# Kernel optimization log

Hardware: AMD Instinct MI355X
Metric: run time of the kernel (lower is better)

The kernel has to match this reference:

```python
import jax, jax.numpy as jnp
import numpy as np

NEG_INF = -9e15  # mask value used by the original module
LEAKY_SLOPE = 0.2


def setup_inputs() -> dict:
    key = jax.random.key(0)
    k1, k2, k3, k4 = jax.random.split(key, 4)
    B, N, F_in = 4, 2048, 128
    H, head_dim = 4, 32
    h = jax.random.normal(k1, (B, N, F_in), dtype=jnp.float32)
    adj = jax.random.randint(k2, (N, N), 0, 2, dtype=jnp.int32)
    W = jax.random.normal(k3, (H, F_in, head_dim), dtype=jnp.float32)
    a = jax.random.normal(k4, (H, 2 * head_dim, 1), dtype=jnp.float32)
    return {"h": h, "adj": adj, "W": W, "a": a}


def reference(h, adj, W, a):
    # h: (B, N, F_in); adj: (N, N) int; W: (H, F_in, D); a: (H, 2D, 1)
    D = W.shape[-1]
    Wh = jnp.einsum('bnf,hfd->bhnd', h, W)          # (B, H, N, D)
    # Original builds [Wh_i || Wh_j] @ a. Split a so that
    # e_ij = Wh_i . a_src + Wh_j . a_dst  (identical math, no N^2*2D concat).
    a_src = a[:, :D, 0]                              # (H, D)
    a_dst = a[:, D:, 0]                              # (H, D)
    e_src = jnp.einsum('bhnd,hd->bhn', Wh, a_src)    # (B, H, N)
    e_dst = jnp.einsum('bhnd,hd->bhn', Wh, a_dst)    # (B, H, N)
    e = jax.nn.leaky_relu(e_src[..., :, None] + e_dst[..., None, :],
                          negative_slope=LEAKY_SLOPE)  # (B, H, N, N)
    masked = jnp.where(adj[None, None] > 0, e, NEG_INF)
    attn = jax.nn.softmax(masked, axis=-1)           # dropout: eval mode (identity)
    out = jnp.einsum('bhij,bhjd->bhid', attn, Wh)    # (B, H, N, D)
    B, H, N, _ = out.shape
    # concat heads along feature dim == transpose to (B, N, H, D) then merge
    return out.transpose(0, 2, 1, 3).reshape(B, N, H * D)
```

## Files before the change

### kernel.cpp

```cpp
#include <hip/hip_runtime.h>
#include <hip/hip_bf16.h>

typedef unsigned short u16;
using f32x4 = __attribute__((ext_vector_type(4))) float;
using short8 = __attribute__((ext_vector_type(8))) short;

constexpr int B_ = 4, N_ = 2048, FIN = 128, H_ = 4, D_ = 32;
constexpr int BH = B_ * H_;
constexpr float LOG2E = 1.4426950408889634f;

static __device__ __forceinline__ float bitsel(int m, float a, unsigned int bu) {
  return __uint_as_float((__float_as_uint(a) & (unsigned)m) | (bu & ~(unsigned)m));
}

constexpr int NPB = 16;

__global__ __launch_bounds__(256) void wh_kernel(
    const float* __restrict__ h, const float* __restrict__ W,
    const float* __restrict__ a, u16* __restrict__ WhT,
    float* __restrict__ es, float* __restrict__ ed) {
  __shared__ float hsh[NPB][FIN];
  __shared__ float part[NPB][H_][D_];
  const int t = threadIdx.x;
  const int fh = t >> 7, hh = (t >> 5) & 3, d = t & 31;

  float Wr[64];
#pragma unroll
  for (int ff = 0; ff < 64; ++ff)
    Wr[ff] = W[hh * (FIN * D_) + (fh * 64 + ff) * D_ + d];

  const int n0 = blockIdx.x * NPB;
  for (int idx = t; idx < NPB * FIN; idx += 256)
    hsh[idx >> 7][idx & 127] = h[(size_t)n0 * FIN + idx];
  __syncthreads();

  float accs[NPB];
#pragma unroll
  for (int r = 0; r < NPB; ++r) {
    float acc = 0.f;
    const float* hr = &hsh[r][fh * 64];
#pragma unroll
    for (int f4 = 0; f4 < 16; ++f4) {
      float4 hv = *(const float4*)(hr + f4 * 4);
      acc += hv.x * Wr[f4 * 4 + 0];
      acc += hv.y * Wr[f4 * 4 + 1];
      acc += hv.z * Wr[f4 * 4 + 2];
      acc += hv.w * Wr[f4 * 4 + 3];
    }
    accs[r] = acc;
  }
  if (fh == 0) {
#pragma unroll
    for (int r = 0; r < NPB; ++r) part[r][hh][d] = accs[r];
  }
  __syncthreads();
  if (fh == 1) {
    const int b = n0 / N_;
    const int bh = b * H_ + hh;
    const int n0r = n0 & (N_ - 1);
    const float asrc = a[hh * 2 * D_ + d];
    const float adst = a[hh * 2 * D_ + D_ + d];
    union { u16 s[16]; uint4 q[2]; } wbuf;
#pragma unroll
    for (int r = 0; r < NPB; ++r) {
      const float wh = accs[r] + part[r][hh][d];
      union { __hip_bfloat16 h; u16 u; } cv;
      cv.h = __float2bfloat16(wh);
      wbuf.s[r] = cv.u;
      float vs = wh * asrc, vd = wh * adst;
#pragma unroll
      for (int o = 16; o >= 1; o >>= 1) {
        vs += __shfl_xor(vs, o, 64);
        vd += __shfl_xor(vd, o, 64);
      }
      if (d == 0) {
        es[(size_t)bh * N_ + n0r + r] = vs * LOG2E;
        ed[(size_t)bh * N_ + n0r + r] = vd * LOG2E;
      }
    }
    u16* dst = WhT + ((size_t)(bh * 32 + d)) * N_ + n0r;
    *(uint4*)dst = wbuf.q[0];
    *(uint4*)(dst + 8) = wbuf.q[1];
  }
}

constexpr int PACKW = N_ * N_ / 64;

__global__ __launch_bounds__(256) void pack_kernel(
    const int* __restrict__ adj, unsigned long long* __restrict__ mask) {
  const int wave = (blockIdx.x * 256 + threadIdx.x) >> 6;
  const int lane = threadIdx.x & 63;
#pragma unroll
  for (int t = 0; t < 8; ++t) {
    const int wdx = wave * 8 + t;
    const int i = wdx >> 5;
    const int jb = (wdx & 31) << 6;
    const int v = adj[(size_t)i * N_ + jb + lane];
    const unsigned long long m = __ballot(v > 0);
    if (lane == 0) mask[wdx] = m;
  }
}

constexpr int ROWS = 16;
constexpr int NSTEP = 16;

__global__ __launch_bounds__(256, 8) void attn_kernel(
    const float* __restrict__ es, const float* __restrict__ ed,
    const u16* __restrict__ WhT, const unsigned int* __restrict__ mask32,
    float* __restrict__ out) {
  __shared__ __align__(16) char arena[12352];
  __shared__ float essh[ROWS], rmsh[ROWS];
  __shared__ float sumsh[4][16];

  float* edsh = (float*)arena;
  unsigned int* maskw = (unsigned int*)(arena + 8192);

  const int bh = blockIdx.x >> 7;
  const int i0 = (blockIdx.x & 127) * ROWS;
  const int tid = threadIdx.x, lane = tid & 63, w = tid >> 6;
  const int jq = w;

  const float* edb = ed + (size_t)bh * N_;
  *(float4*)&edsh[tid * 8] = *(const float4*)(edb + tid * 8);
  *(float4*)&edsh[tid * 8 + 4] = *(const float4*)(edb + tid * 8 + 4);
  const unsigned int* mrow = mask32 + (size_t)i0 * 64;
#pragma unroll
  for (int q = 0; q < 4; ++q) {
    const int idx = tid + q * 256;
    maskw[(idx >> 6) * 65 + (idx & 63)] = mrow[(idx >> 6) * 64 + (idx & 63)];
  }
  if (tid < ROWS) essh[tid] = es[(size_t)bh * N_ + i0 + tid];
  __syncthreads();

  {
    const unsigned int NEGU = __float_as_uint(-3.0e38f);
    float mx0 = -3.0e38f, mx1 = -3.0e38f, mx2 = -3.0e38f, mx3 = -3.0e38f;
    const int l31 = lane & 31, lh = lane >> 5;
#pragma unroll 8
    for (int q = 0; q < 32; ++q) {
      const float edv = edsh[q * 64 + lane];
      const int base = w * 4 * 65 + q * 2 + lh;
      const int b0 = __builtin_amdgcn_sbfe((int)maskw[base], l31, 1);
      const int b1 = __builtin_amdgcn_sbfe((int)maskw[base + 65], l31, 1);
      const int b2 = __builtin_amdgcn_sbfe((int)maskw[base + 130], l31, 1);
      const int b3 = __builtin_amdgcn_sbfe((int)maskw[base + 195], l31, 1);
      mx0 = fmaxf(mx0, bitsel(b0, edv, NEGU));
      mx1 = fmaxf(mx1, bitsel(b1, edv, NEGU));
      mx2 = fmaxf(mx2, bitsel(b2, edv, NEGU));
      mx3 = fmaxf(mx3, bitsel(b3, edv, NEGU));
    }
#pragma unroll
    for (int o = 32; o >= 1; o >>= 1) {
      mx0 = fmaxf(mx0, __shfl_xor(mx0, o, 64));
      mx1 = fmaxf(mx1, __shfl_xor(mx1, o, 64));
      mx2 = fmaxf(mx2, __shfl_xor(mx2, o, 64));
      mx3 = fmaxf(mx3, __shfl_xor(mx3, o, 64));
    }
    if (lane == 0) {
      rmsh[w * 4 + 0] = mx0;
      rmsh[w * 4 + 1] = mx1;
      rmsh[w * 4 + 2] = mx2;
      rmsh[w * 4 + 3] = mx3;
    }
  }
  __syncthreads();

  const int row16 = lane & 15, kg = lane >> 4;
  const float esr = essh[row16];
  const float xm = esr + rmsh[row16];
  const float mxr = fmaxf(xm, 0.2f * xm);
  const float cpos = esr - mxr;
  const float cneg = 0.2f * esr - mxr;

  const unsigned int* mwp = maskw + row16 * 65 + jq * 16;
  const int kg8 = kg << 3;
  unsigned int mreg[16];
#pragma unroll
  for (int s = 0; s < NSTEP; ++s) mreg[s] = mwp[s] >> kg8;

  const u16* wb0 = WhT + ((size_t)(bh * 32 + row16)) * N_ + jq * 512 + kg * 8;
  const u16* wb1 = wb0 + (size_t)16 * N_;
  const float* edq = edsh + jq * 512 + kg * 8;

  short8 ones;
#pragma unroll
  for (int q = 0; q < 8; ++q) ones[q] = (short)0x3F80;

  f32x4 c0 = {}, c1 = {}, csum = {};
  short8 b0 = *(const short8*)wb0;
  short8 b1 = *(const short8*)wb1;

#pragma unroll
  for (int s = 0; s < NSTEP; ++s) {
    const int sn = (s + 1 < NSTEP) ? (s + 1) : s;
    const short8 nb0 = *(const short8*)(wb0 + sn * 32);
    const short8 nb1 = *(const short8*)(wb1 + sn * 32);

    const unsigned int mw = mreg[s];
    const float4 ea = *(const float4*)(edq + s * 32);
    const float4 eb = *(const float4*)(edq + s * 32 + 4);
    const float ev[8] = {ea.x, ea.y, ea.z, ea.w, eb.x, eb.y, eb.z, eb.w};
    float p[8];
#pragma unroll
    for (int j = 0; j < 8; ++j) {
      const float edv = ev[j];
      const float zp = edv + cpos;
      const float zn = __builtin_fmaf(edv, 0.2f, cneg);
      const float z = fmaxf(zp, zn);
      const float e = __builtin_amdgcn_exp2f(z);
      const int mbit = __builtin_amdgcn_sbfe((int)mw, j, 1);
      p[j] = bitsel(mbit, e, 0u);
    }
    union { unsigned int u[4]; short8 v8; } af;
    asm("v_cvt_pk_bf16_f32 %0, %1, %2" : "=v"(af.u[0]) : "v"(p[0]), "v"(p[1]));
    asm("v_cvt_pk_bf16_f32 %0, %1, %2" : "=v"(af.u[1]) : "v"(p[2]), "v"(p[3]));
    asm("v_cvt_pk_bf16_f32 %0, %1, %2" : "=v"(af.u[2]) : "v"(p[4]), "v"(p[5]));
    asm("v_cvt_pk_bf16_f32 %0, %1, %2" : "=v"(af.u[3]) : "v"(p[6]), "v"(p[7]));

    c0 = __builtin_amdgcn_mfma_f32_16x16x32_bf16(af.v8, b0, c0, 0, 0, 0);
    c1 = __builtin_amdgcn_mfma_f32_16x16x32_bf16(af.v8, b1, c1, 0, 0, 0);
    csum = __builtin_amdgcn_mfma_f32_16x16x32_bf16(af.v8, ones, csum, 0, 0, 0);
    b0 = nb0;
    b1 = nb1;
  }

  __syncthreads();

  float* redc = (float*)arena;
#pragma unroll
  for (int r = 0; r < 4; ++r) {
    redc[(jq * 16 + kg * 4 + r) * 33 + row16] = c0[r];
    redc[(jq * 16 + kg * 4 + r) * 33 + 16 + row16] = c1[r];
  }
  if (row16 == 0) {
#pragma unroll
    for (int r = 0; r < 4; ++r) sumsh[jq][kg * 4 + r] = csum[r];
  }
  __syncthreads();

  if (tid < 128) {
    const int r = tid >> 3;
    const int c4 = (tid & 7) * 4;
    const float inv =
        1.f / fmaxf(sumsh[0][r] + sumsh[1][r] + sumsh[2][r] + sumsh[3][r],
                    1e-30f);
    float4 o;
    const float* p0 = &redc[(0 * 16 + r) * 33 + c4];
    const float* p1 = &redc[(1 * 16 + r) * 33 + c4];
    const float* p2 = &redc[(2 * 16 + r) * 33 + c4];
    const float* p3 = &redc[(3 * 16 + r) * 33 + c4];
    o.x = (p0[0] + p1[0] + p2[0] + p3[0]) * inv;
    o.y = (p0[1] + p1[1] + p2[1] + p3[1]) * inv;
    o.z = (p0[2] + p1[2] + p2[2] + p3[2]) * inv;
    o.w = (p0[3] + p1[3] + p2[3] + p3[3]) * inv;
    const int b = bh >> 2, hh = bh & 3;
    *(float4*)&out[((size_t)(b * N_ + i0 + r)) * (H_ * D_) + hh * 32 + c4] = o;
  }
}

extern "C" void kernel_launch(void* const* d_in, const int* in_sizes, int n_in,
                              void* d_out, int out_size, void* d_ws,
                              size_t ws_size, hipStream_t stream) {
  const float* h = (const float*)d_in[0];
  const int* adj = (const int*)d_in[1];
  const float* W = (const float*)d_in[2];
  const float* a = (const float*)d_in[3];
  char* ws = (char*)d_ws;
  u16* WhT = (u16*)ws;
  float* es = (float*)(ws + (2u << 20));
  float* ed = (float*)(ws + (2u << 20) + (128u << 10));
  unsigned long long* mask =
      (unsigned long long*)(ws + (2u << 20) + (256u << 10));
  float* out = (float*)d_out;

  wh_kernel<<<B_ * N_ / NPB, 256, 0, stream>>>(h, W, a, WhT, es, ed);
  pack_kernel<<<PACKW / (8 * 4), 256, 0, stream>>>(adj, mask);
  attn_kernel<<<BH * (N_ / ROWS), 256, 0, stream>>>(
      es, ed, WhT, (const unsigned int*)mask, out);
}
```

Baseline: 124.8 us.

## Deepen B-operand prefetch to two steps and pack score math into float2 ops

```diff
diff --git a/kernel.cpp b/kernel.cpp
--- a/kernel.cpp
+++ b/kernel.cpp
@@ -3,6 +3,7 @@
 
 typedef unsigned short u16;
 using f32x4 = __attribute__((ext_vector_type(4))) float;
+using f32x2 = __attribute__((ext_vector_type(2))) float;
 using short8 = __attribute__((ext_vector_type(8))) short;
 
 constexpr int B_ = 4, N_ = 2048, FIN = 128, H_ = 4, D_ = 32;
@@ -169,14 +170,11 @@
   const float esr = essh[row16];
   const float xm = esr + rmsh[row16];
   const float mxr = fmaxf(xm, 0.2f * xm);
-  const float cpos = esr - mxr;
-  const float cneg = 0.2f * esr - mxr;
+  const f32x2 cpos2 = {esr - mxr, esr - mxr};
+  const f32x2 cneg2 = {0.2f * esr - mxr, 0.2f * esr - mxr};
 
   const unsigned int* mwp = maskw + row16 * 65 + jq * 16;
   const int kg8 = kg << 3;
-  unsigned int mreg[16];
-#pragma unroll
-  for (int s = 0; s < NSTEP; ++s) mreg[s] = mwp[s] >> kg8;
 
   const u16* wb0 = WhT + ((size_t)(bh * 32 + row16)) * N_ + jq * 512 + kg * 8;
   const u16* wb1 = wb0 + (size_t)16 * N_;
@@ -187,29 +185,35 @@
   for (int q = 0; q < 8; ++q) ones[q] = (short)0x3F80;
 
   f32x4 c0 = {}, c1 = {}, csum = {};
-  short8 b0 = *(const short8*)wb0;
-  short8 b1 = *(const short8*)wb1;
+  short8 ba0 = *(const short8*)wb0;
+  short8 ba1 = *(const short8*)wb1;
+  short8 bb0 = *(const short8*)(wb0 + 32);
+  short8 bb1 = *(const short8*)(wb1 + 32);
 
 #pragma unroll
   for (int s = 0; s < NSTEP; ++s) {
-    const int sn = (s + 1 < NSTEP) ? (s + 1) : s;
+    const int sn = (s + 2 < NSTEP) ? (s + 2) : s;
     const short8 nb0 = *(const short8*)(wb0 + sn * 32);
     const short8 nb1 = *(const short8*)(wb1 + sn * 32);
 
-    const unsigned int mw = mreg[s];
+    const unsigned int mw = mwp[s] >> kg8;
     const float4 ea = *(const float4*)(edq + s * 32);
     const float4 eb = *(const float4*)(edq + s * 32 + 4);
-    const float ev[8] = {ea.x, ea.y, ea.z, ea.w, eb.x, eb.y, eb.z, eb.w};
+    const f32x2 ev2[4] = {{ea.x, ea.y}, {ea.z, ea.w}, {eb.x, eb.y}, {eb.z, eb.w}};
     float p[8];
 #pragma unroll
-    for (int j = 0; j < 8; ++j) {
-      const float edv = ev[j];
-      const float zp = edv + cpos;
-      const float zn = __builtin_fmaf(edv, 0.2f, cneg);
-      const float z = fmaxf(zp, zn);
-      const float e = __builtin_amdgcn_exp2f(z);
-      const int mbit = __builtin_amdgcn_sbfe((int)mw, j, 1);
-      p[j] = bitsel(mbit, e, 0u);
+    for (int jj = 0; jj < 4; ++jj) {
+      const f32x2 e2 = ev2[jj];
+      const f32x2 zp = e2 + cpos2;
+      const f32x2 zn = e2 * 0.2f + cneg2;
+      const float z0 = fmaxf(zp.x, zn.x);
+      const float z1 = fmaxf(zp.y, zn.y);
+      const float e0 = __builtin_amdgcn_exp2f(z0);
+      const float e1 = __builtin_amdgcn_exp2f(z1);
+      const int m0 = __builtin_amdgcn_sbfe((int)mw, 2 * jj, 1);
+      const int m1 = __builtin_amdgcn_sbfe((int)mw, 2 * jj + 1, 1);
+      p[2 * jj] = bitsel(m0, e0, 0u);
+      p[2 * jj + 1] = bitsel(m1, e1, 0u);
     }
     union { unsigned int u[4]; short8 v8; } af;
     asm("v_cvt_pk_bf16_f32 %0, %1, %2" : "=v"(af.u[0]) : "v"(p[0]), "v"(p[1]));
@@ -217,11 +221,11 @@
     asm("v_cvt_pk_bf16_f32 %0, %1, %2" : "=v"(af.u[2]) : "v"(p[4]), "v"(p[5]));
     asm("v_cvt_pk_bf16_f32 %0, %1, %2" : "=v"(af.u[3]) : "v"(p[6]), "v"(p[7]));
 
-    c0 = __builtin_amdgcn_mfma_f32_16x16x32_bf16(af.v8, b0, c0, 0, 0, 0);
-    c1 = __builtin_amdgcn_mfma_f32_16x16x32_bf16(af.v8, b1, c1, 0, 0, 0);
+    c0 = __builtin_amdgcn_mfma_f32_16x16x32_bf16(af.v8, ba0, c0, 0, 0, 0);
+    c1 = __builtin_amdgcn_mfma_f32_16x16x32_bf16(af.v8, ba1, c1, 0, 0, 0);
     csum = __builtin_amdgcn_mfma_f32_16x16x32_bf16(af.v8, ones, csum, 0, 0, 0);
-    b0 = nb0;
-    b1 = nb1;
+    ba0 = bb0; ba1 = bb1;
+    bb0 = nb0; bb1 = nb1;
   }
 
   __syncthreads();
```

After: 123.7 us. No clear change (-0.9%).
